# Kernel tuning notes

Measured on AMD Instinct MI355X. Metric: run time of the kernel, lower is better.

Reference implementation:

```python
import jax, jax.numpy as jnp
import numpy as np

B, D, N, S = 4096, 768, 8192, 4  # batch, embedding_dim, len(y)==cat rows, source_size


def setup_inputs() -> dict:
    key = jax.random.key(0)
    k1, k2, k3, k4 = jax.random.split(key, 4)
    batch_x = jax.random.normal(k1, (B, D), dtype=jnp.float32)
    cat = jax.random.normal(k2, (N, D), dtype=jnp.float32)
    y = jax.random.randint(k3, (N,), 0, 2, dtype=jnp.int32)
    # phi_srcs: xavier-uniform-like scale for (D, 1) params, stacked as [S, D]
    phi = jax.random.normal(k4, (S, D), dtype=jnp.float32) * 0.05
    bias = jnp.zeros((1,), dtype=jnp.float32)
    return {"batch_x": batch_x, "cat": cat, "y": y, "phi": phi, "bias": bias}


def reference(batch_x, cat, y, phi, bias):
    # con[n, b] = cat[n] . batch_x[b]   -> [N, B]
    con = jnp.einsum('nd,bd->nb', cat, batch_x)
    # F.normalize(con, p=4, dim=0): divide each column by its 4-norm (eps=1e-12)
    norm4 = jnp.power(jnp.sum(jnp.abs(con) ** 4, axis=0), 0.25)
    con = con / jnp.maximum(norm4, 1e-12)
    # softmax over all N rows (dim=0), per batch column
    con = jax.nn.softmax(con, axis=0)
    # chunk into S sources along the N axis: psi [S, N/S, B]
    psi = con.reshape(S, N // S, B)
    yf = y.astype(jnp.float32).reshape(S, N // S)  # y chunks [S, N/S]
    # theta_s = exp(x @ phi_s): [S, B]  (unnormalized, as in the original output path)
    theta = jnp.exp(jnp.einsum('bd,sd->sb', batch_x, phi))
    # per-source: sum_n y[s,n] * psi[s,n,b], then scale by theta[s,b]; sum over sources
    sum_matrix = jnp.sum(jnp.einsum('sn,snb->sb', yf, psi) * theta, axis=0)  # [B]
    y_hat = jax.nn.sigmoid(sum_matrix + bias)  # bias [1] broadcasts -> [B]
    return y_hat
```

## Files before the change

### kernel.cpp

```cpp
#include <hip/hip_runtime.h>
#include <hip/hip_bf16.h>
#include <stdint.h>
#include <math.h>

#define Bdim 4096
#define Ddim 768
#define Ndim 8192
#define Sdim 4

typedef __attribute__((ext_vector_type(4))) float floatx4;
typedef __attribute__((ext_vector_type(8))) int int8v;
typedef __attribute__((ext_vector_type(4))) int int4v;

__device__ inline int pack_fp8x4(float4 v) {
  int r = __builtin_amdgcn_cvt_pk_fp8_f32(v.x, v.y, 0, 0);
  r = __builtin_amdgcn_cvt_pk_fp8_f32(v.z, v.w, r, 1);
  return r;
}

__device__ __forceinline__ void gl_lds16(const void* g, void* lds_base) {
  __builtin_amdgcn_global_load_lds(
      (const __attribute__((address_space(1))) unsigned int*)g,
      (__attribute__((address_space(3))) unsigned int*)lds_base, 16, 0, 0);
}

__global__ void convert_kernel(const float* __restrict__ x,
                               const float* __restrict__ cat,
                               const float* __restrict__ phi,
                               unsigned char* __restrict__ xq,
                               unsigned char* __restrict__ catq,
                               float* __restrict__ stats,
                               float* __restrict__ theta) {
  int gid = blockIdx.x * blockDim.x + threadIdx.x;
  int stride = gridDim.x * blockDim.x;
  const int nx4 = (Bdim * Ddim) / 4;
  const int nc4 = (Ndim * Ddim) / 4;
  for (int i = gid; i < nx4; i += stride)
    ((int*)xq)[i] = pack_fp8x4(((const float4*)x)[i]);
  for (int i = gid; i < nc4; i += stride)
    ((int*)catq)[i] = pack_fp8x4(((const float4*)cat)[i]);
  if (gid < 6 * Bdim) stats[gid] = 0.0f;

  int gw = gid >> 6;
  int lane = threadIdx.x & 63;
  if (gw < Bdim) {
    const float* xr = x + (size_t)gw * Ddim;
    float a0 = 0.f, a1 = 0.f, a2 = 0.f, a3 = 0.f;
    for (int d = lane; d < Ddim; d += 64) {
      float xv = xr[d];
      a0 = fmaf(xv, phi[d], a0);
      a1 = fmaf(xv, phi[Ddim + d], a1);
      a2 = fmaf(xv, phi[2 * Ddim + d], a2);
      a3 = fmaf(xv, phi[3 * Ddim + d], a3);
    }
#pragma unroll
    for (int off = 32; off > 0; off >>= 1) {
      a0 += __shfl_down(a0, off);
      a1 += __shfl_down(a1, off);
      a2 += __shfl_down(a2, off);
      a3 += __shfl_down(a3, off);
    }
    if (lane == 0) {
      theta[gw] = __expf(a0);
      theta[Bdim + gw] = __expf(a1);
      theta[2 * Bdim + gw] = __expf(a2);
      theta[3 * Bdim + gw] = __expf(a3);
    }
  }
}

__global__ __launch_bounds__(256) void gemm_bt_kernel(
    const unsigned char* __restrict__ A,
    const unsigned char* __restrict__ Bm,
    unsigned int* __restrict__ Cw,
    float* __restrict__ s4) {
  __shared__ unsigned char As[2][128 * 128];
  __shared__ unsigned char Bs[2][128 * 128];

  const int tid = threadIdx.x;
  const int wave = tid >> 6;
  const int lane = tid & 63;
  const int quad = lane >> 4;
  const int l16 = lane & 15;
  const int wm = (wave & 1) * 64;
  const int wn = (wave >> 1) * 64;
  const int m0 = blockIdx.x * 128;
  const int n0 = blockIdx.y * 128;

  floatx4 acc[4][4];
#pragma unroll
  for (int i = 0; i < 4; ++i)
#pragma unroll
    for (int j = 0; j < 4; ++j) acc[i][j] = (floatx4){0.f, 0.f, 0.f, 0.f};

  const unsigned char* a_src[4];
  const unsigned char* b_src[4];
#pragma unroll
  for (int i = 0; i < 4; ++i) {
    int p = tid + 256 * i;
    int row = ((p >> 6) << 3) + (p & 7);
    int colb = ((p >> 3) & 7) * 16;
    a_src[i] = A + (size_t)(m0 + row) * Ddim + colb;
    b_src[i] = Bm + (size_t)(n0 + row) * Ddim + colb;
  }
  const int wbase = (wave * 64) * 16;

#pragma unroll
  for (int i = 0; i < 4; ++i) {
    gl_lds16(a_src[i], &As[0][wbase + i * 4096]);
    gl_lds16(b_src[i], &Bs[0][wbase + i * 4096]);
  }
  __syncthreads();

  int cur = 0;
  for (int kk = 0; kk < 6; ++kk) {
    if (kk < 5) {
      const int k0 = (kk + 1) * 128;
#pragma unroll
      for (int i = 0; i < 4; ++i) {
        gl_lds16(a_src[i] + k0, &As[cur ^ 1][wbase + i * 4096]);
        gl_lds16(b_src[i] + k0, &Bs[cur ^ 1][wbase + i * 4096]);
      }
    }

    int8v af[4], bf[4];
#pragma unroll
    for (int mi = 0; mi < 4; ++mi) {
      int r = wm + mi * 16 + l16;
      int base = ((r >> 3) << 10) + quad * 256 + (r & 7) * 16;
      int4v lo = *(const int4v*)(&As[cur][base]);
      int4v hi = *(const int4v*)(&As[cur][base + 128]);
      af[mi] = __builtin_shufflevector(lo, hi, 0, 1, 2, 3, 4, 5, 6, 7);
    }
#pragma unroll
    for (int ni = 0; ni < 4; ++ni) {
      int r = wn + ni * 16 + l16;
      int base = ((r >> 3) << 10) + quad * 256 + (r & 7) * 16;
      int4v lo = *(const int4v*)(&Bs[cur][base]);
      int4v hi = *(const int4v*)(&Bs[cur][base + 128]);
      bf[ni] = __builtin_shufflevector(lo, hi, 0, 1, 2, 3, 4, 5, 6, 7);
    }
#pragma unroll
    for (int mi = 0; mi < 4; ++mi)
#pragma unroll
      for (int ni = 0; ni < 4; ++ni)
        acc[mi][ni] = __builtin_amdgcn_mfma_scale_f32_16x16x128_f8f6f4(
            af[mi], bf[ni], acc[mi][ni], 0, 0,
            0, 0x7f7f7f7f,
            0, 0x7f7f7f7f);

    __syncthreads();
    cur ^= 1;
  }

  float cs4[4] = {0.f, 0.f, 0.f, 0.f};
#pragma unroll
  for (int mi = 0; mi < 4; ++mi)
#pragma unroll
    for (int ni = 0; ni < 4; ++ni) {
      int g = (m0 + wm + mi * 16) / 4 + quad;
      int col = n0 + wn + ni * 16 + l16;
      floatx4 a = acc[mi][ni];
      int w = __builtin_amdgcn_cvt_pk_fp8_f32(a[0], a[1], 0, 0);
      w = __builtin_amdgcn_cvt_pk_fp8_f32(a[2], a[3], w, 1);
      Cw[(size_t)g * Bdim + col] = (unsigned int)w;
#pragma unroll
      for (int rr = 0; rr < 4; ++rr) {
        float c2 = a[rr] * a[rr];
        cs4[ni] += c2 * c2;
      }
    }
#pragma unroll
  for (int ni = 0; ni < 4; ++ni) {
    float v = cs4[ni];
    v += __shfl_xor(v, 16);
    v += __shfl_xor(v, 32);
    if (quad == 0) atomicAdd(&s4[n0 + wn + ni * 16 + l16], v);
  }
}

__global__ void expsum_kernel(const unsigned int* __restrict__ conq,
                              const float* __restrict__ s4,
                              const int* __restrict__ y,
                              float* __restrict__ denom,
                              float* __restrict__ numer) {
  int b = blockIdx.x * 256 + threadIdx.x;
  int g0 = blockIdx.y * 64;
  int src = (g0 * 4) / (Ndim / Sdim);

  float inv = 1.0f / fmaxf(sqrtf(sqrtf(s4[b])), 1e-12f);
  float inv2 = inv * 1.4426950408889634f;
  const unsigned int* p = conq + (size_t)g0 * Bdim + b;
  float dsum = 0.f, nsum = 0.f;
#pragma unroll 4
  for (int i = 0; i < 64; ++i) {
    unsigned int w = p[(size_t)i * Bdim];
    int4 yv = *(const int4*)(y + 4 * (g0 + i));
    float e0 = exp2f(__builtin_amdgcn_cvt_f32_fp8(w, 0) * inv2);
    float e1 = exp2f(__builtin_amdgcn_cvt_f32_fp8(w, 1) * inv2);
    float e2 = exp2f(__builtin_amdgcn_cvt_f32_fp8(w, 2) * inv2);
    float e3 = exp2f(__builtin_amdgcn_cvt_f32_fp8(w, 3) * inv2);
    dsum += e0 + e1 + e2 + e3;
    nsum += e0 * (float)yv.x + e1 * (float)yv.y + e2 * (float)yv.z +
            e3 * (float)yv.w;
  }
  atomicAdd(&denom[b], dsum);
  atomicAdd(&numer[src * Bdim + b], nsum);
}

__global__ void finalize_kernel(const float* __restrict__ denom,
                                const float* __restrict__ numer,
                                const float* __restrict__ theta,
                                const float* __restrict__ bias,
                                float* __restrict__ out) {
  int b = blockIdx.x * 256 + threadIdx.x;
  float acc = 0.f;
#pragma unroll
  for (int si = 0; si < Sdim; ++si)
    acc += numer[si * Bdim + b] * theta[si * Bdim + b];
  float z = acc / denom[b] + bias[0];
  out[b] = 1.0f / (1.0f + __expf(-z));
}

extern "C" void kernel_launch(void* const* d_in, const int* in_sizes, int n_in,
                              void* d_out, int out_size, void* d_ws,
                              size_t ws_size, hipStream_t stream) {
  const float* batch_x = (const float*)d_in[0];
  const float* cat = (const float*)d_in[1];
  const int* y = (const int*)d_in[2];
  const float* phi = (const float*)d_in[3];
  const float* bias = (const float*)d_in[4];
  float* out = (float*)d_out;

  char* ws = (char*)d_ws;
  unsigned char* catq = (unsigned char*)ws;
  unsigned char* xq = catq + (size_t)Ndim * Ddim;
  unsigned int* conq = (unsigned int*)(xq + (size_t)Bdim * Ddim);
  float* stats = (float*)((unsigned char*)conq + (size_t)Ndim * Bdim);
  float* s4 = stats;
  float* denom = s4 + Bdim;
  float* numer = denom + Bdim;
  float* theta = stats + 6 * Bdim;

  convert_kernel<<<2048, 256, 0, stream>>>(batch_x, cat, phi, xq, catq, stats,
                                           theta);

  dim3 g2(Ndim / 128, Bdim / 128);
  gemm_bt_kernel<<<g2, 256, 0, stream>>>(catq, xq, conq, s4);

  dim3 g3(Bdim / 256, 32);
  expsum_kernel<<<g3, 256, 0, stream>>>(conq, s4, y, denom, numer);

  finalize_kernel<<<Bdim / 256, 256, 0, stream>>>(denom, numer, theta, bias,
                                                  out);
}
```

Baseline: 170.2 us.

## Single-buffer GEMM LDS for occupancy, vectorize theta dot, split expsum finer

The GEMM kernel drops its double-buffered shared memory to a single buffer and sets launch_bounds min blocks to 5. This halves LDS per block so more blocks fit per CU, at the cost of no longer overlapping global-to-LDS loads with MFMA compute (load then sync each k-step). The theta dot product in the convert kernel now uses float4 loads. The expsum kernel uses twice as many blocks, each covering 32 rows, to raise parallelism at the cost of more atomics.

```diff
diff --git a/kernel.cpp b/kernel.cpp
--- a/kernel.cpp
+++ b/kernel.cpp
@@ -44,14 +44,21 @@
   int gw = gid >> 6;
   int lane = threadIdx.x & 63;
   if (gw < Bdim) {
-    const float* xr = x + (size_t)gw * Ddim;
+    const float4* xr4 = (const float4*)(x + (size_t)gw * Ddim);
+    const float4* ph4 = (const float4*)phi;
+    const int D4 = Ddim / 4;
     float a0 = 0.f, a1 = 0.f, a2 = 0.f, a3 = 0.f;
-    for (int d = lane; d < Ddim; d += 64) {
-      float xv = xr[d];
-      a0 = fmaf(xv, phi[d], a0);
-      a1 = fmaf(xv, phi[Ddim + d], a1);
-      a2 = fmaf(xv, phi[2 * Ddim + d], a2);
-      a3 = fmaf(xv, phi[3 * Ddim + d], a3);
+#pragma unroll
+    for (int d4 = lane; d4 < D4; d4 += 64) {
+      float4 xv = xr4[d4];
+      float4 p0 = ph4[d4];
+      float4 p1 = ph4[D4 + d4];
+      float4 p2 = ph4[2 * D4 + d4];
+      float4 p3 = ph4[3 * D4 + d4];
+      a0 = fmaf(xv.x, p0.x, fmaf(xv.y, p0.y, fmaf(xv.z, p0.z, fmaf(xv.w, p0.w, a0))));
+      a1 = fmaf(xv.x, p1.x, fmaf(xv.y, p1.y, fmaf(xv.z, p1.z, fmaf(xv.w, p1.w, a1))));
+      a2 = fmaf(xv.x, p2.x, fmaf(xv.y, p2.y, fmaf(xv.z, p2.z, fmaf(xv.w, p2.w, a2))));
+      a3 = fmaf(xv.x, p3.x, fmaf(xv.y, p3.y, fmaf(xv.z, p3.z, fmaf(xv.w, p3.w, a3))));
     }
 #pragma unroll
     for (int off = 32; off > 0; off >>= 1) {
@@ -69,13 +76,13 @@
   }
 }
 
-__global__ __launch_bounds__(256) void gemm_bt_kernel(
+__global__ __launch_bounds__(256, 5) void gemm_bt_kernel(
     const unsigned char* __restrict__ A,
     const unsigned char* __restrict__ Bm,
     unsigned int* __restrict__ Cw,
     float* __restrict__ s4) {
-  __shared__ unsigned char As[2][128 * 128];
-  __shared__ unsigned char Bs[2][128 * 128];
+  __shared__ unsigned char As[128 * 128];
+  __shared__ unsigned char Bs[128 * 128];
 
   const int tid = threadIdx.x;
   const int wave = tid >> 6;
@@ -107,37 +114,27 @@
 
 #pragma unroll
   for (int i = 0; i < 4; ++i) {
-    gl_lds16(a_src[i], &As[0][wbase + i * 4096]);
-    gl_lds16(b_src[i], &Bs[0][wbase + i * 4096]);
+    gl_lds16(a_src[i], &As[wbase + i * 4096]);
+    gl_lds16(b_src[i], &Bs[wbase + i * 4096]);
   }
   __syncthreads();
 
-  int cur = 0;
   for (int kk = 0; kk < 6; ++kk) {
-    if (kk < 5) {
-      const int k0 = (kk + 1) * 128;
-#pragma unroll
-      for (int i = 0; i < 4; ++i) {
-        gl_lds16(a_src[i] + k0, &As[cur ^ 1][wbase + i * 4096]);
-        gl_lds16(b_src[i] + k0, &Bs[cur ^ 1][wbase + i * 4096]);
-      }
-    }
-
     int8v af[4], bf[4];
 #pragma unroll
     for (int mi = 0; mi < 4; ++mi) {
       int r = wm + mi * 16 + l16;
       int base = ((r >> 3) << 10) + quad * 256 + (r & 7) * 16;
-      int4v lo = *(const int4v*)(&As[cur][base]);
-      int4v hi = *(const int4v*)(&As[cur][base + 128]);
+      int4v lo = *(const int4v*)(&As[base]);
+      int4v hi = *(const int4v*)(&As[base + 128]);
       af[mi] = __builtin_shufflevector(lo, hi, 0, 1, 2, 3, 4, 5, 6, 7);
     }
 #pragma unroll
     for (int ni = 0; ni < 4; ++ni) {
       int r = wn + ni * 16 + l16;
       int base = ((r >> 3) << 10) + quad * 256 + (r & 7) * 16;
-      int4v lo = *(const int4v*)(&Bs[cur][base]);
-      int4v hi = *(const int4v*)(&Bs[cur][base + 128]);
+      int4v lo = *(const int4v*)(&Bs[base]);
+      int4v hi = *(const int4v*)(&Bs[base + 128]);
       bf[ni] = __builtin_shufflevector(lo, hi, 0, 1, 2, 3, 4, 5, 6, 7);
     }
 #pragma unroll
@@ -150,7 +147,16 @@
             0, 0x7f7f7f7f);
 
     __syncthreads();
-    cur ^= 1;
+
+    if (kk < 5) {
+      const int k0 = (kk + 1) * 128;
+#pragma unroll
+      for (int i = 0; i < 4; ++i) {
+        gl_lds16(a_src[i] + k0, &As[wbase + i * 4096]);
+        gl_lds16(b_src[i] + k0, &Bs[wbase + i * 4096]);
+      }
+      __syncthreads();
+    }
   }
 
   float cs4[4] = {0.f, 0.f, 0.f, 0.f};
@@ -185,7 +191,7 @@
                               float* __restrict__ denom,
                               float* __restrict__ numer) {
   int b = blockIdx.x * 256 + threadIdx.x;
-  int g0 = blockIdx.y * 64;
+  int g0 = blockIdx.y * 32;
   int src = (g0 * 4) / (Ndim / Sdim);
 
   float inv = 1.0f / fmaxf(sqrtf(sqrtf(s4[b])), 1e-12f);
@@ -193,7 +199,7 @@
   const unsigned int* p = conq + (size_t)g0 * Bdim + b;
   float dsum = 0.f, nsum = 0.f;
 #pragma unroll 4
-  for (int i = 0; i < 64; ++i) {
+  for (int i = 0; i < 32; ++i) {
     unsigned int w = p[(size_t)i * Bdim];
     int4 yv = *(const int4*)(y + 4 * (g0 + i));
     float e0 = exp2f(__builtin_amdgcn_cvt_f32_fp8(w, 0) * inv2);
@@ -248,7 +254,7 @@
   dim3 g2(Ndim / 128, Bdim / 128);
   gemm_bt_kernel<<<g2, 256, 0, stream>>>(catq, xq, conq, s4);
 
-  dim3 g3(Bdim / 256, 32);
+  dim3 g3(Bdim / 256, 64);
   expsum_kernel<<<g3, 256, 0, stream>>>(conq, s4, y, denom, numer);
 
   finalize_kernel<<<Bdim / 256, 256, 0, stream>>>(denom, numer, theta, bias,
```

After: 259.2 us. 1.52x slower.
